# Performance work log

Measured on AMD Instinct MI355X. Metric: run time of the kernel, lower is better.

## Reference

```python
import jax, jax.numpy as jnp
import numpy as np

B, N, H, NH = 2, 1024, 1024, 16  # batch, seq per branch, hidden, heads


def setup_inputs() -> dict:
    key = jax.random.key(0)
    k1, k2, k3, k4 = jax.random.split(key, 4)
    x = jax.random.normal(k1, (B, N, H), jnp.float32)
    x2 = jax.random.normal(k2, (B, N, H), jnp.float32)
    w_qkv = jax.random.normal(k3, (3 * H, H), jnp.float32) * 0.02  # nn.Linear(H, 3H), no bias
    w_out = jax.random.normal(k4, (H, H), jnp.float32) * 0.02
    b_out = jnp.zeros((H,), jnp.float32)
    return {"x": x, "x2": x2, "w_qkv": w_qkv, "w_out": w_out, "b_out": b_out, "num_heads": NH}


def _qkv_split(x, w_qkv, nh):
    # qkv Linear then Rearrange 'b n (qkv l d) -> qkv b l n d'
    b, n, h = x.shape
    d = h // nh
    qkv = x @ w_qkv.T                                    # [b, n, 3h]
    qkv = qkv.reshape(b, n, 3, nh, d).transpose(2, 0, 3, 1, 4)  # [3, b, nh, n, d]
    return qkv[0], qkv[1], qkv[2]


def reference(x, x2, w_qkv, w_out, b_out, num_heads):
    nh = num_heads
    d = x.shape[-1] // nh
    scale = float(d) ** -0.5
    q, k, v = _qkv_split(x, w_qkv, nh)
    q2, k2, v2 = _qkv_split(x2, w_qkv, nh)
    # cross-branch concat along seq dim
    q = jnp.concatenate([q, q2], axis=2)
    k = jnp.concatenate([k, k2], axis=2)
    v = jnp.concatenate([v, v2], axis=2)
    att = jax.nn.softmax(jnp.einsum('bhxd,bhyd->bhxy', q, k) * scale, axis=-1)  # [b,nh,2N,2N]
    o = jnp.einsum('bhxy,bhyd->bhxd', att, v)            # [b,nh,2N,d]
    o1, o2 = jnp.split(o, 2, axis=2)

    def proj(o):
        b, h, n, dd = o.shape
        o = o.transpose(0, 2, 1, 3).reshape(b, n, h * dd)  # 'b h l d -> b l (h d)'
        return o @ w_out.T + b_out

    return proj(o1), proj(o2)
```

## Files before the change

kernel.cpp:

```cpp
#include <hip/hip_runtime.h>
#include <hip/hip_bf16.h>

#define NB      2
#define NSEQ    1024
#define S2      2048
#define HDIM    1024
#define NHEADS  16
#define DHEAD   64
#define Q_SCALE 0.18033688011112042f

typedef unsigned short ushort_t;
typedef __attribute__((ext_vector_type(8))) short short8;
typedef __attribute__((ext_vector_type(4))) float f32x4;
typedef __attribute__((ext_vector_type(16))) float f32x16;

__device__ __forceinline__ ushort_t f2bf(float f) {
    union { float f; unsigned int u; } c; c.f = f;
    unsigned int u = c.u;
    u += 0x7FFFu + ((u >> 16) & 1u);
    return (ushort_t)(u >> 16);
}

__device__ __forceinline__ unsigned pack_bf16x2(float a, float b) {
    union { __hip_bfloat162 h; unsigned u; } cv;
    cv.h = __float22bfloat162_rn(float2{a, b});
    return cv.u;
}

__global__ __launch_bounds__(256) void cvt_all(
    const float* __restrict__ x, const float* __restrict__ x2,
    const float* __restrict__ wqkv, const float* __restrict__ wout,
    ushort_t* __restrict__ Xb, ushort_t* __restrict__ Wqb, ushort_t* __restrict__ Wob)
{
    int b = blockIdx.x;
    const float* s; ushort_t* d; int i;
    if (b < 2048)      { s = x;    d = Xb;            i = b * 256 + threadIdx.x; }
    else if (b < 4096) { s = x2;   d = Xb + 2097152;  i = (b - 2048) * 256 + threadIdx.x; }
    else if (b < 7168) { s = wqkv; d = Wqb;           i = (b - 4096) * 256 + threadIdx.x; }
    else               { s = wout; d = Wob;           i = (b - 7168) * 256 + threadIdx.x; }
    float4 v = ((const float4*)s)[i];
    ushort4 o; o.x = f2bf(v.x); o.y = f2bf(v.y); o.z = f2bf(v.z); o.w = f2bf(v.w);
    ((ushort4*)d)[i] = o;
}

__global__ __launch_bounds__(256) void qkv_gemm_mfma(
    const ushort_t* __restrict__ Xb, const ushort_t* __restrict__ Wqb,
    ushort_t* __restrict__ Qb, ushort_t* __restrict__ Kb, ushort_t* __restrict__ Vtb)
{
    __shared__ ushort_t As[2 * 128 * 32];
    __shared__ ushort_t Bs[2 * 128 * 32];
    __shared__ float    Sc[4][16 * 20];
    const int t = threadIdx.x;
    const int lane = t & 63, quad = lane >> 4, l15 = lane & 15;
    const int w = t >> 6;
    const int wm = (w >> 1) * 64, wn = (w & 1) * 64;
    const int r0 = blockIdx.y * 128, c0 = blockIdx.x * 128;

    const int g_chunk = (lane & 3) ^ ((lane >> 3) & 3);
    const int srow_lo = w * 16 + (lane >> 2);

    auto stage = [&](int k0, int buf) {
        #pragma unroll
        for (int p = 0; p < 2; ++p) {
            int row = srow_lo + p * 64;
            const ushort_t* gpA = Xb  + (size_t)(r0 + row) * HDIM + k0 + g_chunk * 8;
            const ushort_t* gpB = Wqb + (size_t)(c0 + row) * HDIM + k0 + g_chunk * 8;
            ushort_t* lpA = As + buf * 4096 + p * 2048 + w * 512;
            ushort_t* lpB = Bs + buf * 4096 + p * 2048 + w * 512;
            __builtin_amdgcn_global_load_lds(
                (const __attribute__((address_space(1))) void*)gpA,
                (__attribute__((address_space(3))) void*)lpA, 16, 0, 0);
            __builtin_amdgcn_global_load_lds(
                (const __attribute__((address_space(1))) void*)gpB,
                (__attribute__((address_space(3))) void*)lpB, 16, 0, 0);
        }
    };

    f32x4 acc[4][4];
    #pragma unroll
    for (int i = 0; i < 4; ++i)
        #pragma unroll
        for (int j = 0; j < 4; ++j) acc[i][j] = (f32x4){0.f, 0.f, 0.f, 0.f};

    stage(0, 0);
    stage(32, 1);
    __syncthreads();

    const int sw = (l15 >> 1) & 3;
    for (int it = 0; it < 32; ++it) {
        const ushort_t* a = As + (it & 1) * 4096;
        const ushort_t* b = Bs + (it & 1) * 4096;
        short8 af[4], bf[4];
        #pragma unroll
        for (int mi = 0; mi < 4; ++mi) {
            int ra = wm + mi * 16 + l15;
            af[mi] = *(const short8*)(a + ra * 32 + ((quad ^ sw) * 8));
        }
        #pragma unroll
        for (int ni = 0; ni < 4; ++ni) {
            int rb = wn + ni * 16 + l15;
            bf[ni] = *(const short8*)(b + rb * 32 + ((quad ^ sw) * 8));
        }
        #pragma unroll
        for (int mi = 0; mi < 4; ++mi)
            #pragma unroll
            for (int ni = 0; ni < 4; ++ni)
                acc[mi][ni] = __builtin_amdgcn_mfma_f32_16x16x32_bf16(af[mi], bf[ni], acc[mi][ni], 0, 0, 0);
        __syncthreads();
        if (it < 30) stage((it + 2) * 32, it & 1);
    }

    const int branch = r0 >> 11;
    const int bb     = (r0 & 2047) >> 10;
    const int qi     = c0 >> 10;
    float* sc = &Sc[w][0];

    if (qi == 2) {
        #pragma unroll
        for (int mi = 0; mi < 4; ++mi) {
            int sbase = branch * NSEQ + (r0 & 1023) + wm + mi * 16 + quad * 4;
            #pragma unroll
            for (int ni = 0; ni < 4; ++ni) {
                int cc = (c0 & 1023) + wn + ni * 16;
                int h  = cc >> 6;
                int dd = (cc & 63) + l15;
                ushort4 pv;
                pv.x = f2bf(acc[mi][ni][0]); pv.y = f2bf(acc[mi][ni][1]);
                pv.z = f2bf(acc[mi][ni][2]); pv.w = f2bf(acc[mi][ni][3]);
                *(ushort4*)(Vtb + ((size_t)(bb * NHEADS + h) * DHEAD + dd) * S2 + sbase) = pv;
            }
        }
    } else {
        const float qsc = (qi == 0) ? Q_SCALE : 1.0f;
        ushort_t* base = (qi ? Kb : Qb);
        const int row = lane >> 2, ch = lane & 3;
        #pragma unroll
        for (int mi = 0; mi < 4; ++mi) {
            int sb = branch * NSEQ + (r0 & 1023) + wm + mi * 16;
            #pragma unroll
            for (int ni = 0; ni < 4; ++ni) {
                int cc = (c0 & 1023) + wn + ni * 16;
                int h  = cc >> 6;
                int db = cc & 63;
                #pragma unroll
                for (int reg = 0; reg < 4; ++reg)
                    sc[(quad * 4 + reg) * 20 + l15] = acc[mi][ni][reg] * qsc;
                float4 v = *(const float4*)&sc[row * 20 + ch * 4];
                uint2 pk;
                pk.x = pack_bf16x2(v.x, v.y);
                pk.y = pack_bf16x2(v.z, v.w);
                *(uint2*)(base + ((size_t)(bb * NHEADS + h) * S2 + sb + row) * DHEAD + db + ch * 4) = pk;
            }
        }
    }
}

__global__ __launch_bounds__(256) void attn_mfma(
    const ushort_t* __restrict__ Qb, const ushort_t* __restrict__ Kb,
    const ushort_t* __restrict__ Vtb, ushort_t* __restrict__ Ob)
{
    __shared__ ushort_t Ks[4 * 64 * 64];
    __shared__ ushort_t Vs[4 * 64 * 64];

    const int t = threadIdx.x, lane = t & 63, w = t >> 6;
    const int l31 = lane & 31, hi = lane >> 5;

    const int id  = blockIdx.x;
    const int j   = id >> 3;
    const int bh  = ((j & 3) << 3) | (id & 7);
    const int r0  = (j >> 2) * 128;

    const ushort_t* Qh  = Qb  + (size_t)bh * S2 * DHEAD;
    const ushort_t* Kh  = Kb  + (size_t)bh * S2 * DHEAD;
    const ushort_t* Vth = Vtb + (size_t)bh * DHEAD * S2;

    const int slot = lane & 7;
    const int rsub = lane >> 3;
    auto prefetch = [&](int kt_, int buf_) {
        #pragma unroll
        for (int c = 0; c < 2; ++c) {
            int row = w * 16 + c * 8 + rsub;
            int g   = slot ^ (row & 7);
            const ushort_t* gpK = Kh  + (size_t)(kt_ * 64 + row) * DHEAD + g * 8;
            const ushort_t* gpV = Vth + (size_t)row * S2 + kt_ * 64 + g * 8;
            ushort_t* lpK = &Ks[buf_ * 4096 + w * 1024 + c * 512];
            ushort_t* lpV = &Vs[buf_ * 4096 + w * 1024 + c * 512];
            __builtin_amdgcn_global_load_lds(
                (const __attribute__((address_space(1))) void*)gpK,
                (__attribute__((address_space(3))) void*)lpK, 16, 0, 0);
            __builtin_amdgcn_global_load_lds(
                (const __attribute__((address_space(1))) void*)gpV,
                (__attribute__((address_space(3))) void*)lpV, 16, 0, 0);
        }
    };

    short8 aq[4];
    {
        const ushort_t* qp = Qh + (size_t)(r0 + 32 * w + l31) * DHEAD + hi * 8;
        #pragma unroll
        for (int sd = 0; sd < 4; ++sd) aq[sd] = *(const short8*)(qp + sd * 16);
    }

    const int s7 = l31 & 7;
    int offA[4];
    #pragma unroll
    for (int s = 0; s < 4; ++s)
        offA[s] = (l31 * 64 + (((s * 2 + hi) ^ s7) * 8)) * 2;

    f32x16 oacc0, oacc1;
    #pragma unroll
    for (int i = 0; i < 16; ++i) { oacc0[i] = 0.f; oacc1[i] = 0.f; }
    float la0 = 0.f, la1 = 0.f, la2 = 0.f, la3 = 0.f;

    prefetch(0, 0);
    prefetch(1, 1);
    prefetch(2, 2);
    asm volatile("s_waitcnt vmcnt(4)" ::: "memory");
    __builtin_amdgcn_s_barrier();
    __builtin_amdgcn_sched_barrier(0);

    auto qk_tile = [&](const char* kb, f32x16& d0, f32x16& d1) {
        #pragma unroll
        for (int i = 0; i < 16; ++i) { d0[i] = 0.f; d1[i] = 0.f; }
        __builtin_amdgcn_s_setprio(1);
        #pragma unroll
        for (int sd = 0; sd < 4; ++sd) {
            short8 k0 = *(const short8*)(kb + offA[sd]);
            short8 k1 = *(const short8*)(kb + offA[sd] + 4096);
            d0 = __builtin_amdgcn_mfma_f32_32x32x16_bf16(k0, aq[sd], d0, 0, 0, 0);
            d1 = __builtin_amdgcn_mfma_f32_32x32x16_bf16(k1, aq[sd], d1, 0, 0, 0);
        }
        __builtin_amdgcn_s_setprio(0);
    };

    f32x16 sA0, sA1, sB0, sB1;
    qk_tile((const char*)Ks, sA0, sA1);

    auto tile_body = [&](f32x16& c0, f32x16& c1, f32x16& n0, f32x16& n1, int kt) {
        if (kt < 31)
            qk_tile((const char*)Ks + ((kt + 1) & 3) * 8192, n0, n1);

        unsigned pw[4][4];
        #pragma unroll
        for (int half = 0; half < 2; ++half) {
            float p[8], q[8];
            #pragma unroll
            for (int jj = 0; jj < 8; ++jj) {
                p[jj] = __builtin_exp2f(c0[half * 8 + jj]);
                q[jj] = __builtin_exp2f(c1[half * 8 + jj]);
            }
            la0 += p[0] + p[4]; la1 += p[1] + p[5];
            la2 += p[2] + p[6]; la3 += p[3] + p[7];
            la0 += q[0] + q[4]; la1 += q[1] + q[5];
            la2 += q[2] + q[6]; la3 += q[3] + q[7];

            unsigned a0 = pack_bf16x2(p[0], p[1]), b0 = pack_bf16x2(p[2], p[3]);
            unsigned c0_ = pack_bf16x2(p[4], p[5]), d0_ = pack_bf16x2(p[6], p[7]);
            asm("v_permlane32_swap_b32 %0, %1" : "+v"(a0), "+v"(c0_));
            asm("v_permlane32_swap_b32 %0, %1" : "+v"(b0), "+v"(d0_));
            pw[half][0] = a0; pw[half][1] = b0; pw[half][2] = c0_; pw[half][3] = d0_;

            unsigned a1 = pack_bf16x2(q[0], q[1]), b1 = pack_bf16x2(q[2], q[3]);
            unsigned c1_ = pack_bf16x2(q[4], q[5]), d1_ = pack_bf16x2(q[6], q[7]);
            asm("v_permlane32_swap_b32 %0, %1" : "+v"(a1), "+v"(c1_));
            asm("v_permlane32_swap_b32 %0, %1" : "+v"(b1), "+v"(d1_));
            pw[2 + half][0] = a1; pw[2 + half][1] = b1; pw[2 + half][2] = c1_; pw[2 + half][3] = d1_;
        }

        const char* vb = (const char*)Vs + (kt & 3) * 8192;
        __builtin_amdgcn_s_setprio(1);
        #pragma unroll
        for (int sk = 0; sk < 4; ++sk) {
            union { unsigned u[4]; short8 s8; } pa;
            pa.u[0] = pw[sk][0]; pa.u[1] = pw[sk][1];
            pa.u[2] = pw[sk][2]; pa.u[3] = pw[sk][3];
            short8 v0 = *(const short8*)(vb + offA[sk]);
            short8 v1 = *(const short8*)(vb + offA[sk] + 4096);
            oacc0 = __builtin_amdgcn_mfma_f32_32x32x16_bf16(pa.s8, v0, oacc0, 0, 0, 0);
            oacc1 = __builtin_amdgcn_mfma_f32_32x32x16_bf16(pa.s8, v1, oacc1, 0, 0, 0);
        }
        __builtin_amdgcn_s_setprio(0);

        if (kt <= 28) {
            prefetch(kt + 3, (kt + 3) & 3);
            asm volatile("s_waitcnt vmcnt(4)" ::: "memory");
            __builtin_amdgcn_s_barrier();
            __builtin_amdgcn_sched_barrier(0);
        } else if (kt == 29) {
            asm volatile("s_waitcnt vmcnt(0)" ::: "memory");
            __builtin_amdgcn_s_barrier();
            __builtin_amdgcn_sched_barrier(0);
        }
    };

    #pragma unroll 1
    for (int kt = 0; kt < 32; kt += 2) {
        tile_body(sA0, sA1, sB0, sB1, kt);
        tile_body(sB0, sB1, sA0, sA1, kt + 1);
    }

    float l = (la0 + la1) + (la2 + la3);
    l += __shfl_xor(l, 32);
    const float inv = 1.0f / l;

    ushort_t* obase = Ob + (size_t)bh * S2 * DHEAD;
    #pragma unroll
    for (int r = 0; r < 16; ++r) {
        const int ql = (r & 3) + 8 * (r >> 2) + 4 * hi;
        const float iv = __shfl(inv, ql);
        const size_t rowoff = (size_t)(r0 + 32 * w + ql) * DHEAD;
        obase[rowoff + l31]      = f2bf(oacc0[r] * iv);
        obase[rowoff + 32 + l31] = f2bf(oacc1[r] * iv);
    }
}

__global__ __launch_bounds__(256) void proj_gemm_mfma(
    const ushort_t* __restrict__ Ob, const ushort_t* __restrict__ Wob,
    const float* __restrict__ Bo, float* __restrict__ Out)
{
    __shared__ ushort_t As[2 * 128 * 32];
    __shared__ ushort_t Bs[2 * 64 * 32];
    __shared__ float    Sc[4][16 * 20];
    const int t = threadIdx.x;
    const int lane = t & 63, quad = lane >> 4, l15 = lane & 15;
    const int w = t >> 6;
    const int wm = (w >> 1) * 64, wn = (w & 1) * 32;
    const int r0 = blockIdx.y * 128, c0 = blockIdx.x * 64;
    const int branch = r0 >> 11, bb = (r0 & 2047) >> 10;

    const int g_chunk = (lane & 3) ^ ((lane >> 3) & 3);
    const int srow_lo = w * 16 + (lane >> 2);

    auto stage = [&](int k0, int buf) {
        int h = k0 >> 6, off = k0 & 63;
        const ushort_t* gpB = Wob + (size_t)(c0 + srow_lo) * HDIM + k0 + g_chunk * 8;
        ushort_t* lpB = Bs + buf * 2048 + w * 512;
        __builtin_amdgcn_global_load_lds(
            (const __attribute__((address_space(1))) void*)gpB,
            (__attribute__((address_space(3))) void*)lpB, 16, 0, 0);
        #pragma unroll
        for (int p = 0; p < 2; ++p) {
            int row = srow_lo + p * 64;
            int s = branch * NSEQ + (r0 & 1023) + row;
            const ushort_t* gpA = Ob + ((size_t)(bb * NHEADS + h) * S2 + s) * DHEAD + off + g_chunk * 8;
            ushort_t* lpA = As + buf * 4096 + p * 2048 + w * 512;
            __builtin_amdgcn_global_load_lds(
                (const __attribute__((address_space(1))) void*)gpA,
                (__attribute__((address_space(3))) void*)lpA, 16, 0, 0);
        }
    };

    f32x4 acc[4][2];
    #pragma unroll
    for (int i = 0; i < 4; ++i)
        #pragma unroll
        for (int j = 0; j < 2; ++j) acc[i][j] = (f32x4){0.f, 0.f, 0.f, 0.f};

    stage(0, 0);
    stage(32, 1);
    __syncthreads();

    const int sw = (l15 >> 1) & 3;
    for (int it = 0; it < 32; ++it) {
        const ushort_t* a = As + (it & 1) * 4096;
        const ushort_t* b = Bs + (it & 1) * 2048;
        short8 af[4], bf[2];
        #pragma unroll
        for (int mi = 0; mi < 4; ++mi) {
            int ra = wm + mi * 16 + l15;
            af[mi] = *(const short8*)(a + ra * 32 + ((quad ^ sw) * 8));
        }
        #pragma unroll
        for (int ni = 0; ni < 2; ++ni) {
            int rb = wn + ni * 16 + l15;
            bf[ni] = *(const short8*)(b + rb * 32 + ((quad ^ sw) * 8));
        }
        #pragma unroll
        for (int mi = 0; mi < 4; ++mi)
            #pragma unroll
            for (int ni = 0; ni < 2; ++ni)
                acc[mi][ni] = __builtin_amdgcn_mfma_f32_16x16x32_bf16(af[mi], bf[ni], acc[mi][ni], 0, 0, 0);
        __syncthreads();
        if (it < 30) stage((it + 2) * 32, it & 1);
    }

    float* sc = &Sc[w][0];
    const int row = lane >> 2, ch = lane & 3;
    #pragma unroll
    for (int mi = 0; mi < 4; ++mi) {
        int rb0 = r0 + wm + mi * 16;
        #pragma unroll
        for (int ni = 0; ni < 2; ++ni) {
            int cb = c0 + wn + ni * 16;
            #pragma unroll
            for (int reg = 0; reg < 4; ++reg)
                sc[(quad * 4 + reg) * 20 + l15] = acc[mi][ni][reg];
            float4 v = *(const float4*)&sc[row * 20 + ch * 4];
            float4 bias = *(const float4*)&Bo[cb + ch * 4];
            v.x += bias.x; v.y += bias.y; v.z += bias.z; v.w += bias.w;
            *(float4*)&Out[(size_t)(rb0 + row) * HDIM + cb + ch * 4] = v;
        }
    }
}

extern "C" void kernel_launch(void* const* d_in, const int* in_sizes, int n_in,
                              void* d_out, int out_size, void* d_ws, size_t ws_size,
                              hipStream_t stream) {
    const float* x    = (const float*)d_in[0];
    const float* x2   = (const float*)d_in[1];
    const float* wqkv = (const float*)d_in[2];
    const float* wout = (const float*)d_in[3];
    const float* bout = (const float*)d_in[4];
    float* out = (float*)d_out;

    char* ws = (char*)d_ws;
    ushort_t* Xb  = (ushort_t*)(ws);
    ushort_t* Wqb = (ushort_t*)(ws + (8u  << 20));
    ushort_t* Wob = (ushort_t*)(ws + (14u << 20));
    ushort_t* Qb  = (ushort_t*)(ws + (16u << 20));
    ushort_t* Kb  = (ushort_t*)(ws + (24u << 20));
    ushort_t* Vtb = (ushort_t*)(ws + (32u << 20));
    ushort_t* Ob  = (ushort_t*)(ws + (40u << 20));

    cvt_all<<<8192, 256, 0, stream>>>(x, x2, wqkv, wout, Xb, Wqb, Wob);
    qkv_gemm_mfma<<<dim3(24, 32), 256, 0, stream>>>(Xb, Wqb, Qb, Kb, Vtb);
    attn_mfma<<<512, 256, 0, stream>>>(Qb, Kb, Vtb, Ob);
    proj_gemm_mfma<<<dim3(16, 32), 256, 0, stream>>>(Ob, Wob, bout, out);
}
```

Before: 205.8 us.

## Split attention KV range across two blocks and combine partial outputs

Splits each attention query tile's key range in half, launching twice as many blocks. Each block writes unnormalized bf16 partial outputs and row sums, and a new combine kernel adds the halves and normalizes. LDS buffering drops from 4 to 2 stages with occupancy hint 4, aiming to fill more CUs on a 512-block grid. The cost is an extra kernel launch, extra global traffic for partials, and bf16 rounding of unnormalized partials. Softmax uses no max subtraction, so summing partials is exact in principle.

Result: slower. 362.5 us (+76.2%).

```diff
diff --git a/kernel.cpp b/kernel.cpp
--- a/kernel.cpp
+++ b/kernel.cpp
@@ -19,6 +19,11 @@
     unsigned int u = c.u;
     u += 0x7FFFu + ((u >> 16) & 1u);
     return (ushort_t)(u >> 16);
+}
+
+__device__ __forceinline__ float bf2f(ushort_t u) {
+    union { unsigned int u; float f; } c; c.u = ((unsigned int)u) << 16;
+    return c.f;
 }
 
 __device__ __forceinline__ unsigned pack_bf16x2(float a, float b) {
@@ -155,20 +160,24 @@
     }
 }
 
-__global__ __launch_bounds__(256) void attn_mfma(
+__global__ __launch_bounds__(256, 4) void attn_mfma(
     const ushort_t* __restrict__ Qb, const ushort_t* __restrict__ Kb,
-    const ushort_t* __restrict__ Vtb, ushort_t* __restrict__ Ob)
+    const ushort_t* __restrict__ Vtb, ushort_t* __restrict__ Op0,
+    ushort_t* __restrict__ Op1, float* __restrict__ Lp)
 {
-    __shared__ ushort_t Ks[4 * 64 * 64];
-    __shared__ ushort_t Vs[4 * 64 * 64];
+    __shared__ ushort_t Ks[2 * 64 * 64];
+    __shared__ ushort_t Vs[2 * 64 * 64];
 
     const int t = threadIdx.x, lane = t & 63, w = t >> 6;
     const int l31 = lane & 31, hi = lane >> 5;
 
-    const int id  = blockIdx.x;
-    const int j   = id >> 3;
-    const int bh  = ((j & 3) << 3) | (id & 7);
-    const int r0  = (j >> 2) * 128;
+    const int id   = blockIdx.x;
+    const int j    = id >> 3;
+    const int bh   = ((j & 3) << 3) | (id & 7);
+    const int j2   = j >> 2;
+    const int r0   = (j2 & 15) << 7;
+    const int half = j2 >> 4;
+    const int kts  = half * 16;
 
     const ushort_t* Qh  = Qb  + (size_t)bh * S2 * DHEAD;
     const ushort_t* Kh  = Kb  + (size_t)bh * S2 * DHEAD;
@@ -212,13 +221,6 @@
     for (int i = 0; i < 16; ++i) { oacc0[i] = 0.f; oacc1[i] = 0.f; }
     float la0 = 0.f, la1 = 0.f, la2 = 0.f, la3 = 0.f;
 
-    prefetch(0, 0);
-    prefetch(1, 1);
-    prefetch(2, 2);
-    asm volatile("s_waitcnt vmcnt(4)" ::: "memory");
-    __builtin_amdgcn_s_barrier();
-    __builtin_amdgcn_sched_barrier(0);
-
     auto qk_tile = [&](const char* kb, f32x16& d0, f32x16& d1) {
         #pragma unroll
         for (int i = 0; i < 16; ++i) { d0[i] = 0.f; d1[i] = 0.f; }
@@ -233,21 +235,31 @@
         __builtin_amdgcn_s_setprio(0);
     };
 
+    prefetch(kts, 0);
+    prefetch(kts + 1, 1);
+    asm volatile("s_waitcnt vmcnt(4)" ::: "memory");
+    __builtin_amdgcn_s_barrier();
+    __builtin_amdgcn_sched_barrier(0);
+
     f32x16 sA0, sA1, sB0, sB1;
     qk_tile((const char*)Ks, sA0, sA1);
 
-    auto tile_body = [&](f32x16& c0, f32x16& c1, f32x16& n0, f32x16& n1, int kt) {
-        if (kt < 31)
-            qk_tile((const char*)Ks + ((kt + 1) & 3) * 8192, n0, n1);
+    auto tile_body = [&](f32x16& c0, f32x16& c1, f32x16& n0, f32x16& n1, int i) {
+        if (i < 15) {
+            asm volatile("s_waitcnt vmcnt(0)" ::: "memory");
+            __builtin_amdgcn_s_barrier();
+            __builtin_amdgcn_sched_barrier(0);
+            qk_tile((const char*)Ks + ((i + 1) & 1) * 8192, n0, n1);
+        }
 
         unsigned pw[4][4];
         #pragma unroll
-        for (int half = 0; half < 2; ++half) {
+        for (int halfp = 0; halfp < 2; ++halfp) {
             float p[8], q[8];
             #pragma unroll
             for (int jj = 0; jj < 8; ++jj) {
-                p[jj] = __builtin_exp2f(c0[half * 8 + jj]);
-                q[jj] = __builtin_exp2f(c1[half * 8 + jj]);
+                p[jj] = __builtin_exp2f(c0[halfp * 8 + jj]);
+                q[jj] = __builtin_exp2f(c1[halfp * 8 + jj]);
             }
             la0 += p[0] + p[4]; la1 += p[1] + p[5];
             la2 += p[2] + p[6]; la3 += p[3] + p[7];
@@ -258,16 +270,16 @@
             unsigned c0_ = pack_bf16x2(p[4], p[5]), d0_ = pack_bf16x2(p[6], p[7]);
             asm("v_permlane32_swap_b32 %0, %1" : "+v"(a0), "+v"(c0_));
             asm("v_permlane32_swap_b32 %0, %1" : "+v"(b0), "+v"(d0_));
-            pw[half][0] = a0; pw[half][1] = b0; pw[half][2] = c0_; pw[half][3] = d0_;
+            pw[halfp][0] = a0; pw[halfp][1] = b0; pw[halfp][2] = c0_; pw[halfp][3] = d0_;
 
             unsigned a1 = pack_bf16x2(q[0], q[1]), b1 = pack_bf16x2(q[2], q[3]);
             unsigned c1_ = pack_bf16x2(q[4], q[5]), d1_ = pack_bf16x2(q[6], q[7]);
             asm("v_permlane32_swap_b32 %0, %1" : "+v"(a1), "+v"(c1_));
             asm("v_permlane32_swap_b32 %0, %1" : "+v"(b1), "+v"(d1_));
-            pw[2 + half][0] = a1; pw[2 + half][1] = b1; pw[2 + half][2] = c1_; pw[2 + half][3] = d1_;
-        }
-
-        const char* vb = (const char*)Vs + (kt & 3) * 8192;
+            pw[2 + halfp][0] = a1; pw[2 + halfp][1] = b1; pw[2 + halfp][2] = c1_; pw[2 + halfp][3] = d1_;
+        }
+
+        const char* vb = (const char*)Vs + (i & 1) * 8192;
         __builtin_amdgcn_s_setprio(1);
         #pragma unroll
         for (int sk = 0; sk < 4; ++sk) {
@@ -281,37 +293,48 @@
         }
         __builtin_amdgcn_s_setprio(0);
 
-        if (kt <= 28) {
-            prefetch(kt + 3, (kt + 3) & 3);
-            asm volatile("s_waitcnt vmcnt(4)" ::: "memory");
+        if (i <= 13) {
             __builtin_amdgcn_s_barrier();
-            __builtin_amdgcn_sched_barrier(0);
-        } else if (kt == 29) {
-            asm volatile("s_waitcnt vmcnt(0)" ::: "memory");
-            __builtin_amdgcn_s_barrier();
-            __builtin_amdgcn_sched_barrier(0);
+            prefetch(kts + i + 2, i & 1);
         }
     };
 
     #pragma unroll 1
-    for (int kt = 0; kt < 32; kt += 2) {
-        tile_body(sA0, sA1, sB0, sB1, kt);
-        tile_body(sB0, sB1, sA0, sA1, kt + 1);
+    for (int i = 0; i < 16; i += 2) {
+        tile_body(sA0, sA1, sB0, sB1, i);
+        tile_body(sB0, sB1, sA0, sA1, i + 1);
     }
 
     float l = (la0 + la1) + (la2 + la3);
     l += __shfl_xor(l, 32);
-    const float inv = 1.0f / l;
-
-    ushort_t* obase = Ob + (size_t)bh * S2 * DHEAD;
+    const size_t rowb = (size_t)bh * S2 + r0 + 32 * w;
+    if (hi == 0) Lp[(size_t)half * (32 * S2) + rowb + l31] = l;
+
+    ushort_t* obase = (half ? Op1 : Op0) + rowb * DHEAD;
     #pragma unroll
     for (int r = 0; r < 16; ++r) {
         const int ql = (r & 3) + 8 * (r >> 2) + 4 * hi;
-        const float iv = __shfl(inv, ql);
-        const size_t rowoff = (size_t)(r0 + 32 * w + ql) * DHEAD;
-        obase[rowoff + l31]      = f2bf(oacc0[r] * iv);
-        obase[rowoff + 32 + l31] = f2bf(oacc1[r] * iv);
-    }
+        const size_t rowoff = (size_t)ql * DHEAD;
+        obase[rowoff + l31]      = f2bf(oacc0[r]);
+        obase[rowoff + 32 + l31] = f2bf(oacc1[r]);
+    }
+}
+
+__global__ __launch_bounds__(256) void combine_o(
+    const ushort_t* __restrict__ Op1, const float* __restrict__ Lp,
+    ushort_t* __restrict__ Ob )
+{
+    int idx = blockIdx.x * 256 + threadIdx.x;
+    int e   = idx * 8;
+    int row = e >> 6;
+    float inv = 1.0f / (Lp[row] + Lp[32 * S2 + row]);
+    union { short8 v; ushort_t u[8]; } a, b, o;
+    a.v = *(const short8*)(Ob + e);
+    b.v = *(const short8*)(Op1 + e);
+    #pragma unroll
+    for (int jj = 0; jj < 8; ++jj)
+        o.u[jj] = f2bf((bf2f(a.u[jj]) + bf2f(b.u[jj])) * inv);
+    *(short8*)(Ob + e) = o.v;
 }
 
 __global__ __launch_bounds__(256) void proj_gemm_mfma(
@@ -420,10 +443,13 @@
     ushort_t* Qb  = (ushort_t*)(ws + (16u << 20));
     ushort_t* Kb  = (ushort_t*)(ws + (24u << 20));
     ushort_t* Vtb = (ushort_t*)(ws + (32u << 20));
-    ushort_t* Ob  = (ushort_t*)(ws + (40u << 20));
+    ushort_t* Op0 = (ushort_t*)(ws);
+    float*    Lp  = (float*)   (ws + (8u  << 20));
+    ushort_t* Op1 = (ushort_t*)(ws + (40u << 20));
 
     cvt_all<<<8192, 256, 0, stream>>>(x, x2, wqkv, wout, Xb, Wqb, Wob);
     qkv_gemm_mfma<<<dim3(24, 32), 256, 0, stream>>>(Xb, Wqb, Qb, Kb, Vtb);
-    attn_mfma<<<512, 256, 0, stream>>>(Qb, Kb, Vtb, Ob);
-    proj_gemm_mfma<<<dim3(16, 32), 256, 0, stream>>>(Ob, Wob, bout, out);
-}
+    attn_mfma<<<1024, 256, 0, stream>>>(Qb, Kb, Vtb, Op0, Op1, Lp);
+    combine_o<<<2048, 256, 0, stream>>>(Op1, Lp, Op0);
+    proj_gemm_mfma<<<dim3(16, 32), 256, 0, stream>>>(Op0, Wob, bout, out);
+}
```
